# Kernel optimization log

Measured on AMD Instinct MI355X. Metric: run time of the kernel, lower is better.

Reference implementation:

```python
import jax, jax.numpy as jnp
import numpy as np

N, E, G = 50000, 800000, 64
L, C, IN, H, OUT = 3, 4, 64, 64, 64
BN_EPS = 1e-5


def setup_inputs() -> dict:
    key = jax.random.key(0)
    ks = jax.random.split(key, 12)
    x = jax.random.normal(ks[0], (N, IN), dtype=jnp.float32)
    cluster_labels = jax.random.randint(ks[1], (N,), 0, C, dtype=jnp.int32)
    edge_index = jax.random.randint(ks[2], (2, E), 0, N, dtype=jnp.int64)
    batch = jnp.sort(jax.random.randint(ks[3], (N,), 0, G, dtype=jnp.int64))
    s1 = 1.0 / np.sqrt(H)
    # per (layer, cluster) GIN MLP params: Lin(H,H) -> BN -> ReLU -> Lin(H,H)
    W1 = jax.random.normal(ks[4], (L, C, H, H), dtype=jnp.float32) * s1
    b1 = jnp.zeros((L, C, H), dtype=jnp.float32)
    g1 = jnp.ones((L, C, H), dtype=jnp.float32)
    be1 = jnp.zeros((L, C, H), dtype=jnp.float32)
    W2 = jax.random.normal(ks[5], (L, C, H, H), dtype=jnp.float32) * s1
    b2 = jnp.zeros((L, C, H), dtype=jnp.float32)
    # pool MLP: Lin(H*L, H) -> BN -> ReLU -> Lin(H, OUT)
    Wp1 = jax.random.normal(ks[6], (H * L, H), dtype=jnp.float32) / np.sqrt(H * L)
    bp1 = jnp.zeros((H,), dtype=jnp.float32)
    gp = jnp.ones((H,), dtype=jnp.float32)
    bep = jnp.zeros((H,), dtype=jnp.float32)
    Wp2 = jax.random.normal(ks[7], (H, OUT), dtype=jnp.float32) * s1
    bp2 = jnp.zeros((OUT,), dtype=jnp.float32)
    return {"x": x, "cluster_labels": cluster_labels, "edge_index": edge_index,
            "batch": batch, "W1": W1, "b1": b1, "g1": g1, "be1": be1,
            "W2": W2, "b2": b2, "Wp1": Wp1, "bp1": bp1, "gp": gp,
            "bep": bep, "Wp2": Wp2, "bp2": bp2}


def _masked_bn(h, mf, gamma, beta):
    # BatchNorm computed only over rows where mask is set (those are the rows fed to nn)
    cnt = jnp.maximum(mf.sum(), 1.0)
    mean = (mf[:, None] * h).sum(0) / cnt
    var = (mf[:, None] * (h - mean) ** 2).sum(0) / cnt
    return (h - mean) * jax.lax.rsqrt(var + BN_EPS) * gamma + beta


def _bn(h, gamma, beta):
    mean = h.mean(0)
    var = ((h - mean) ** 2).mean(0)
    return (h - mean) * jax.lax.rsqrt(var + BN_EPS) * gamma + beta


def reference(x, cluster_labels, edge_index, batch, W1, b1, g1, be1, W2, b2,
              Wp1, bp1, gp, bep, Wp2, bp2):
    src, dst = edge_index[0], edge_index[1]
    pooled = []
    for t in range(L):
        for c in range(C):
            mask = cluster_labels == c
            mf = mask.astype(x.dtype)
            # GIN aggregation: out[i] = sum_{j -> i} x[j]
            agg = jax.ops.segment_sum(x[src], dst, num_segments=N)
            h = agg + x  # (1 + eps) * x residual with eps = 0
            h = h @ W1[t, c] + b1[t, c]
            h = jax.nn.relu(_masked_bn(h, mf, g1[t, c], be1[t, c]))
            h = h @ W2[t, c] + b2[t, c]
            x = jnp.where(mask[:, None], h, x)
        pooled.append(jax.ops.segment_sum(x, batch, num_segments=G))
    z = jnp.concatenate(pooled, axis=1)  # [G, H*L]
    z = z @ Wp1 + bp1
    z = jax.nn.relu(_bn(z, gp, bep))
    return z @ Wp2 + bp2
```

## Files before the change

### kernel.cpp

```cpp
#include <hip/hip_runtime.h>
#include <hip/hip_bf16.h>

#define NN 50000
#define EE 800000
#define GG 64
#define LL 3
#define CC 4
#define HH 64
#define BN_EPS 1e-5f
#define NSHADOW 4
#define SBLK 196
#define GIN_BLOCKS 2048
#define MM_BLOCKS 256
#define ECHUNKS 3125
#define NODE_RANGE 6250
#define TMAX 2
#define H1STRIDE 80


typedef __attribute__((ext_vector_type(8))) short bf16x8;
typedef __attribute__((ext_vector_type(4))) float f32x4;

__device__ __forceinline__ float bf2f(short s) {
    return __int_as_float(((int)(unsigned short)s) << 16);
}
__device__ __forceinline__ short f2bf(float v) {
    __hip_bfloat16 hb = __float2bfloat16(v);
    return *(short*)&hb;
}


__global__ void k_deghist(const int* __restrict__ dst, int* __restrict__ deg,
                          const int* __restrict__ labels, int* __restrict__ blockcnt,
                          const float* __restrict__ x_in, __hip_bfloat16* __restrict__ xw,
                          const float* __restrict__ W1, const float* __restrict__ W2,
                          short* __restrict__ wf) {
    __shared__ int cnt[CC];
    int tid = threadIdx.x;
    for (int i = blockIdx.x * 256 + tid; i < NN * 64; i += gridDim.x * 256)
        xw[i] = __float2bfloat16(x_in[i]);
    int o = blockIdx.x * 256 + tid;
    if (o < 24 * 4096) {
        int m = o >> 12;
        int r = o & 4095;
        int colt = r >> 10;
        int fragk = (r >> 9) & 1;
        int lane = (r >> 3) & 63;
        int j = r & 7;
        int k = fragk * 32 + ((lane >> 4) << 3) + j;
        int n = colt * 16 + (lane & 15);
        const float* src = (m < 12) ? (W1 + (size_t)m * 4096) : (W2 + (size_t)(m - 12) * 4096);
        wf[o] = f2bf(src[k * 64 + n]);
    }
    bool hist = (blockIdx.x < SBLK);
    if (hist && tid < CC) cnt[tid] = 0;
    __syncthreads();
    int gid = blockIdx.x * 256 + tid;
    if (gid < EE) atomicAdd(&deg[dst[gid]], 1);
    if (hist && gid < NN) atomicAdd(&cnt[labels[gid]], 1);
    __syncthreads();
    if (hist && tid < CC) blockcnt[tid * SBLK + blockIdx.x] = cnt[tid];
}

__global__ __launch_bounds__(256) void k_scancombo(
    const int* __restrict__ deg, int* __restrict__ rowptr, int* __restrict__ dpart,
    const int* __restrict__ blockcnt, int* __restrict__ coffs, int* __restrict__ ccount) {
    __shared__ int smem[CC * 256];
    int tid = threadIdx.x;
    if (blockIdx.x < SBLK) {
        int i = blockIdx.x * 256 + tid;
        int v = (i < NN) ? deg[i] : 0;
        smem[tid] = v;
        __syncthreads();
        for (int off = 1; off < 256; off <<= 1) {
            int u = (tid >= off) ? smem[tid - off] : 0;
            __syncthreads();
            smem[tid] += u;
            __syncthreads();
        }
        if (i < NN) rowptr[i] = smem[tid] - v;
        if (tid == 255) dpart[blockIdx.x] = smem[255];
    } else {
        int own[CC];
        for (int c = 0; c < CC; c++) {
            own[c] = (tid < SBLK) ? blockcnt[c * SBLK + tid] : 0;
            smem[c * 256 + tid] = own[c];
        }
        __syncthreads();
        for (int off = 1; off < 256; off <<= 1) {
            int v[CC];
            for (int c = 0; c < CC; c++) v[c] = (tid >= off) ? smem[c * 256 + tid - off] : 0;
            __syncthreads();
            for (int c = 0; c < CC; c++) smem[c * 256 + tid] += v[c];
            __syncthreads();
        }
        if (tid < SBLK)
            for (int c = 0; c < CC; c++) coffs[c * SBLK + tid] = smem[c * 256 + tid] - own[c];
        if (tid == 0)
            for (int c = 0; c < CC; c++) ccount[c] = smem[c * 256 + 255];
    }
}

__global__ __launch_bounds__(256) void k_dscan2(int* __restrict__ dpart,
                                                int* __restrict__ dbase,
                                                int* __restrict__ rowptr) {
    __shared__ int s[256];
    int tid = threadIdx.x;
    int v = (tid < SBLK) ? dpart[tid] : 0;
    s[tid] = v;
    __syncthreads();
    for (int off = 1; off < 256; off <<= 1) {
        int u = (tid >= off) ? s[tid - off] : 0;
        __syncthreads();
        s[tid] += u;
        __syncthreads();
    }
    if (tid < SBLK) dbase[tid] = s[tid] - v;
    if (tid == 0) rowptr[NN] = EE;
}

__global__ __launch_bounds__(256) void k_cfill_dscan3(
    int* __restrict__ rowptr, const int* __restrict__ dbase, int* __restrict__ cursor,
    const int* __restrict__ labels, const int* __restrict__ coffs, int* __restrict__ clist) {
    __shared__ int pos[CC];
    int tid = threadIdx.x;
    if (tid < CC) pos[tid] = coffs[tid * SBLK + blockIdx.x];
    __syncthreads();
    int i = blockIdx.x * 256 + tid;
    if (i < NN) {
        int r = rowptr[i] + dbase[blockIdx.x];
        rowptr[i] = r;
        cursor[i] = r;
        int c = labels[i];
        int p = atomicAdd(&pos[c], 1);
        clist[c * NN + p] = i;
    }
}

__global__ void k_fill(const int* __restrict__ src, const int* __restrict__ dst,
                       int* __restrict__ cursor, int* __restrict__ adj) {
    int range = blockIdx.x / ECHUNKS;
    int e = (blockIdx.x - range * ECHUNKS) * 256 + threadIdx.x;
    if (e < EE) {
        int d = dst[e];
        int lo = range * NODE_RANGE;
        if (d >= lo && d < lo + NODE_RANGE) {
            int pos = atomicAdd(&cursor[d], 1);
            adj[pos] = src[e] << 7;
        }
    }
}

__global__ __launch_bounds__(256) void k_gather(
    const __hip_bfloat16* __restrict__ xw, const int* __restrict__ adj,
    const int* __restrict__ rowptr, const int* __restrict__ clist_c,
    const int* __restrict__ ccount_c, __hip_bfloat16* __restrict__ aggbuf,
    const int* __restrict__ batch, float* __restrict__ z, int tpool) {
    int cnt = *ccount_c;
    int lane = threadIdx.x & 63;
    int wave = threadIdx.x >> 6;
    int wid = blockIdx.x * 4 + wave;
    int nwaves = gridDim.x * 4;
    int grp = lane >> 4;
    int l16 = lane & 15;
    const char* xwb = (const char*)xw;
    int idx = wid;
    int node_next = (idx < cnt) ? clist_c[idx] : 0;
    for (; idx < cnt; idx += nwaves) {
        int node = node_next;
        int nidx = idx + nwaves;
        if (nidx < cnt) node_next = clist_c[nidx];
        int rb = rowptr[node], re = rowptr[node + 1];
        float ax[8], ay[8], az[8], aw[8];
        #pragma unroll
        for (int u = 0; u < 8; u++) { ax[u] = 0.f; ay[u] = 0.f; az[u] = 0.f; aw[u] = 0.f; }
        if (grp == 0) {
            uint2 v = *(const uint2*)(xwb + ((size_t)node << 7) + l16 * 8);
            ax[0] += __int_as_float((int)(v.x << 16));
            ay[0] += __int_as_float((int)(v.x & 0xffff0000u));
            az[0] += __int_as_float((int)(v.y << 16));
            aw[0] += __int_as_float((int)(v.y & 0xffff0000u));
        }
        int base = rb, rem = re - rb;
        while (rem > 0) {
            int take = min(rem, 64);
            int nb = adj[base + min(lane, take - 1)];
            int j = 0;
            for (; j + 32 <= take; j += 32) {
                #pragma unroll
                for (int u = 0; u < 8; u++) {
                    int o = __shfl(nb, j + u * 4 + grp);
                    uint2 v = *(const uint2*)(xwb + o + l16 * 8);
                    ax[u] += __int_as_float((int)(v.x << 16));
                    ay[u] += __int_as_float((int)(v.x & 0xffff0000u));
                    az[u] += __int_as_float((int)(v.y << 16));
                    aw[u] += __int_as_float((int)(v.y & 0xffff0000u));
                }
            }
            for (; j + 16 <= take; j += 16) {
                #pragma unroll
                for (int u = 0; u < 4; u++) {
                    int o = __shfl(nb, j + u * 4 + grp);
                    uint2 v = *(const uint2*)(xwb + o + l16 * 8);
                    ax[u] += __int_as_float((int)(v.x << 16));
                    ay[u] += __int_as_float((int)(v.x & 0xffff0000u));
                    az[u] += __int_as_float((int)(v.y << 16));
                    aw[u] += __int_as_float((int)(v.y & 0xffff0000u));
                }
            }
            for (; j < take; j += 4) {
                int e = j + grp;
                int o = __shfl(nb, min(e, take - 1));
                if (e < take) {
                    uint2 v = *(const uint2*)(xwb + o + l16 * 8);
                    ax[0] += __int_as_float((int)(v.x << 16));
                    ay[0] += __int_as_float((int)(v.x & 0xffff0000u));
                    az[0] += __int_as_float((int)(v.y << 16));
                    aw[0] += __int_as_float((int)(v.y & 0xffff0000u));
                }
            }
            base += take; rem -= take;
        }
        float X = ((ax[0] + ax[1]) + (ax[2] + ax[3])) + ((ax[4] + ax[5]) + (ax[6] + ax[7]));
        float Y = ((ay[0] + ay[1]) + (ay[2] + ay[3])) + ((ay[4] + ay[5]) + (ay[6] + ay[7]));
        float Z = ((az[0] + az[1]) + (az[2] + az[3])) + ((az[4] + az[5]) + (az[6] + az[7]));
        float W = ((aw[0] + aw[1]) + (aw[2] + aw[3])) + ((aw[4] + aw[5]) + (aw[6] + aw[7]));
        X += __shfl_xor(X, 16); X += __shfl_xor(X, 32);
        Y += __shfl_xor(Y, 16); Y += __shfl_xor(Y, 32);
        Z += __shfl_xor(Z, 16); Z += __shfl_xor(Z, 32);
        W += __shfl_xor(W, 16); W += __shfl_xor(W, 32);
        if (grp == 0) {
            ushort4 st;
            st.x = (unsigned short)f2bf(X);
            st.y = (unsigned short)f2bf(Y);
            st.z = (unsigned short)f2bf(Z);
            st.w = (unsigned short)f2bf(W);
            *(ushort4*)((char*)aggbuf + ((size_t)idx << 7) + l16 * 8) = st;
        }
    }
    if (tpool >= 0) {
        int lo = wid * 64;
        if (lo < NN) {
            int hi = min(lo + 64, NN);
            float acc = 0.f;
            int curg = batch[lo];
            for (int n = lo; n < hi; n++) {
                int g = batch[n];
                if (g != curg) {
                    atomicAdd(&z[curg * (HH * LL) + tpool * HH + lane], acc);
                    acc = 0.f;
                    curg = g;
                }
                acc += __bfloat162float(xw[(size_t)n * 64 + lane]);
            }
            atomicAdd(&z[curg * (HH * LL) + tpool * HH + lane], acc);
        }
    }
}

__global__ __launch_bounds__(256) void k_mlp(
    __hip_bfloat16* __restrict__ xw, const __hip_bfloat16* __restrict__ aggbuf,
    const int* __restrict__ clist_c, const int* __restrict__ ccount_c,
    const short* __restrict__ wf1, const float* __restrict__ b1c,
    const float* __restrict__ g1c, const float* __restrict__ be1c,
    const short* __restrict__ wf2, const float* __restrict__ b2c,
    float* __restrict__ bnacc, int* __restrict__ barcnt) {
    __shared__ __align__(16) short h1s[4 * TMAX * 16 * H1STRIDE];
    __shared__ float lds_scale[64];
    __shared__ float lds_shift[64];
    int cnt = *ccount_c;
    int tiles = (cnt + 15) >> 4;
    int lane = threadIdx.x & 63;
    int wave = threadIdx.x >> 6;
    int wid = blockIdx.x * 4 + wave;
    int nwaves = gridDim.x * 4;
    int quad = lane >> 4;
    int l15 = lane & 15;
    short* myh1 = h1s + wave * (TMAX * 16 * H1STRIDE);

    bf16x8 wb[8];
    #pragma unroll
    for (int f = 0; f < 8; f++)
        wb[f] = *(const bf16x8*)(wf1 + f * 512 + lane * 8);
    float bcol[4];
    #pragma unroll
    for (int colt = 0; colt < 4; colt++) bcol[colt] = b1c[colt * 16 + l15];

    float sS[4] = {0.f, 0.f, 0.f, 0.f};
    float sQ[4] = {0.f, 0.f, 0.f, 0.f};
    {
        int nt = 0;
        for (int tile = wid; tile < tiles && nt < TMAX; tile += nwaves, nt++) {
            int tb = tile << 4;
            int row = tb + l15;
            const __hip_bfloat16* ar = aggbuf + (size_t)row * 64 + quad * 8;
            bf16x8 a0 = *(const bf16x8*)ar;
            bf16x8 a1 = *(const bf16x8*)(ar + 32);
            short* slot = myh1 + nt * (16 * H1STRIDE);
            #pragma unroll
            for (int colt = 0; colt < 4; colt++) {
                f32x4 acc = {0.f, 0.f, 0.f, 0.f};
                acc = __builtin_amdgcn_mfma_f32_16x16x32_bf16(a0, wb[colt * 2 + 0], acc, 0, 0, 0);
                acc = __builtin_amdgcn_mfma_f32_16x16x32_bf16(a1, wb[colt * 2 + 1], acc, 0, 0, 0);
                #pragma unroll
                for (int r = 0; r < 4; r++) {
                    int nrow = tb + quad * 4 + r;
                    float s = acc[r] + bcol[colt];
                    short hb = f2bf(s);
                    slot[(quad * 4 + r) * H1STRIDE + colt * 16 + l15] = hb;
                    if (nrow < cnt) {
                        float st = bf2f(hb);
                        sS[colt] += st;
                        sQ[colt] += st * st;
                    }
                }
            }
        }
    }
    #pragma unroll
    for (int colt = 0; colt < 4; colt++) {
        sS[colt] += __shfl_xor(sS[colt], 16); sS[colt] += __shfl_xor(sS[colt], 32);
        sQ[colt] += __shfl_xor(sQ[colt], 16); sQ[colt] += __shfl_xor(sQ[colt], 32);
    }
    if (quad == 0) {
        int slot = (blockIdx.x & (NSHADOW - 1)) * 128;
        #pragma unroll
        for (int colt = 0; colt < 4; colt++) {
            atomicAdd(&bnacc[slot + colt * 16 + l15], sS[colt]);
            atomicAdd(&bnacc[slot + 64 + colt * 16 + l15], sQ[colt]);
        }
    }
    __syncthreads();
    if (threadIdx.x == 0) {
        __hip_atomic_fetch_add(barcnt, 1, __ATOMIC_RELEASE, __HIP_MEMORY_SCOPE_AGENT);
        while (__hip_atomic_load(barcnt, __ATOMIC_ACQUIRE, __HIP_MEMORY_SCOPE_AGENT) < MM_BLOCKS)
            __builtin_amdgcn_s_sleep(2);
    }
    __syncthreads();
    if (threadIdx.x < 64) {
        float s = 0.f, q = 0.f;
        #pragma unroll
        for (int sh = 0; sh < NSHADOW; sh++) {
            s += __hip_atomic_load(&bnacc[sh * 128 + threadIdx.x],
                                   __ATOMIC_RELAXED, __HIP_MEMORY_SCOPE_AGENT);
            q += __hip_atomic_load(&bnacc[sh * 128 + 64 + threadIdx.x],
                                   __ATOMIC_RELAXED, __HIP_MEMORY_SCOPE_AGENT);
        }
        float fc = fmaxf((float)cnt, 1.f);
        float mean = s / fc;
        float var = q / fc - mean * mean;
        float sc = g1c[threadIdx.x] * rsqrtf(var + BN_EPS);
        lds_scale[threadIdx.x] = sc;
        lds_shift[threadIdx.x] = be1c[threadIdx.x] - mean * sc;
    }
    __syncthreads();
    #pragma unroll
    for (int f = 0; f < 8; f++)
        wb[f] = *(const bf16x8*)(wf2 + f * 512 + lane * 8);
    #pragma unroll
    for (int colt = 0; colt < 4; colt++) bcol[colt] = b2c[colt * 16 + l15];
    float scl0[8], sft0[8], scl1[8], sft1[8];
    #pragma unroll
    for (int j = 0; j < 8; j++) {
        int ch = quad * 8 + j;
        scl0[j] = lds_scale[ch];      sft0[j] = lds_shift[ch];
        scl1[j] = lds_scale[ch + 32]; sft1[j] = lds_shift[ch + 32];
    }
    {
        int nt = 0;
        for (int tile = wid; tile < tiles && nt < TMAX; tile += nwaves, nt++) {
            int tb = tile << 4;
            const short* slot = myh1 + nt * (16 * H1STRIDE);
            const short* hr = slot + l15 * H1STRIDE + quad * 8;
            bf16x8 h0 = *(const bf16x8*)hr;
            bf16x8 h1f = *(const bf16x8*)(hr + 32);
            bf16x8 a0, a1;
            #pragma unroll
            for (int j = 0; j < 8; j++) {
                a0[j] = f2bf(fmaxf(bf2f(h0[j]) * scl0[j] + sft0[j], 0.f));
                a1[j] = f2bf(fmaxf(bf2f(h1f[j]) * scl1[j] + sft1[j], 0.f));
            }
            #pragma unroll
            for (int colt = 0; colt < 4; colt++) {
                f32x4 acc = {0.f, 0.f, 0.f, 0.f};
                acc = __builtin_amdgcn_mfma_f32_16x16x32_bf16(a0, wb[colt * 2 + 0], acc, 0, 0, 0);
                acc = __builtin_amdgcn_mfma_f32_16x16x32_bf16(a1, wb[colt * 2 + 1], acc, 0, 0, 0);
                #pragma unroll
                for (int r = 0; r < 4; r++) {
                    int nrow = tb + quad * 4 + r;
                    if (nrow < cnt) {
                        int node = clist_c[nrow];
                        xw[(size_t)node * 64 + colt * 16 + l15] =
                            __float2bfloat16(acc[r] + bcol[colt]);
                    }
                }
            }
        }
    }
}

__global__ void k_pool(const __hip_bfloat16* __restrict__ xw, const int* __restrict__ batch,
                       float* __restrict__ z, int t) {
    const int CHUNK = 64;
    int lane = threadIdx.x & 63;
    int wg = (blockIdx.x * blockDim.x + threadIdx.x) >> 6;
    int lo = wg * CHUNK;
    if (lo >= NN) return;
    int hi = min(lo + CHUNK, NN);
    float acc = 0.f;
    int curg = batch[lo];
    for (int n = lo; n < hi; n++) {
        int g = batch[n];
        if (g != curg) {
            atomicAdd(&z[curg * (HH * LL) + t * HH + lane], acc);
            acc = 0.f;
            curg = g;
        }
        acc += __bfloat162float(xw[(size_t)n * 64 + lane]);
    }
    atomicAdd(&z[curg * (HH * LL) + t * HH + lane], acc);
}

__global__ __launch_bounds__(256) void k_final1(
    const float* __restrict__ z, const float* __restrict__ Wp1,
    const float* __restrict__ bp1, float* __restrict__ hbuf) {
    __shared__ float red[256];
    int g = blockIdx.x;
    int k = threadIdx.x & 63;
    int part = threadIdx.x >> 6;
    float s = 0.f;
    #pragma unroll 8
    for (int j = part * 48; j < (part + 1) * 48; j++)
        s += z[g * (HH * LL) + j] * Wp1[j * 64 + k];
    red[threadIdx.x] = s;
    __syncthreads();
    if (part == 0)
        hbuf[g * 64 + k] = red[k] + red[64 + k] + red[128 + k] + red[192 + k] + bp1[k];
}

__global__ __launch_bounds__(256) void k_final2(
    const float* __restrict__ hbuf, const float* __restrict__ gp,
    const float* __restrict__ bep, const float* __restrict__ Wp2,
    const float* __restrict__ bp2, float* __restrict__ out) {
    __shared__ float lds[64 * 64];
    __shared__ float sscale[64];
    __shared__ float sshift[64];
    int tid = threadIdx.x;
    for (int i = tid; i < 64 * 64; i += 256) lds[i] = hbuf[i];
    __syncthreads();
    if (tid < 64) {
        float s = 0.f, q = 0.f;
        for (int g = 0; g < 64; g++) { float v = lds[g * 64 + tid]; s += v; q += v * v; }
        float mean = s / 64.f;
        float var = q / 64.f - mean * mean;
        float sc = gp[tid] * rsqrtf(var + BN_EPS);
        sscale[tid] = sc;
        sshift[tid] = bep[tid] - mean * sc;
    }
    __syncthreads();
    for (int i = tid; i < 64 * 64; i += 256) {
        int k = i & 63;
        lds[i] = fmaxf(lds[i] * sscale[k] + sshift[k], 0.f);
    }
    __syncthreads();
    for (int i = tid; i < 64 * 64; i += 256) {
        int g = i >> 6, o = i & 63;
        float s = bp2[o];
        #pragma unroll 8
        for (int k = 0; k < 64; k++) s += lds[g * 64 + k] * Wp2[k * 64 + o];
        out[g * 64 + o] = s;
    }
}

extern "C" void kernel_launch(void* const* d_in, const int* in_sizes, int n_in,
                              void* d_out, int out_size, void* d_ws, size_t ws_size,
                              hipStream_t stream) {
    const float* x_in = (const float*)d_in[0];
    const int* labels = (const int*)d_in[1];
    const int* esrc = (const int*)d_in[2];
    const int* edst = esrc + EE;
    const int* batch = (const int*)d_in[3];
    const float* W1 = (const float*)d_in[4];
    const float* b1 = (const float*)d_in[5];
    const float* g1 = (const float*)d_in[6];
    const float* be1 = (const float*)d_in[7];
    const float* W2 = (const float*)d_in[8];
    const float* b2 = (const float*)d_in[9];
    const float* Wp1 = (const float*)d_in[10];
    const float* bp1 = (const float*)d_in[11];
    const float* gp = (const float*)d_in[12];
    const float* bep = (const float*)d_in[13];
    const float* Wp2 = (const float*)d_in[14];
    const float* bp2 = (const float*)d_in[15];
    float* out = (float*)d_out;

    char* p = (char*)d_ws;
    auto carve = [&](size_t bytes) -> void* {
        void* r = (void*)p;
        p += (bytes + 255) & ~(size_t)255;
        return r;
    };
    float* bnacc = (float*)carve((size_t)LL * CC * NSHADOW * 128 * 4);
    float* z     = (float*)carve((size_t)GG * HH * LL * 4);
    int*   deg   = (int*)carve((size_t)NN * 4);
    int*   barcnt= (int*)carve((size_t)16 * 4);
    size_t zero_bytes = (size_t)(p - (char*)d_ws);
    int*   ccount  = (int*)carve(CC * 4);
    int*   blockcnt= (int*)carve((size_t)CC * SBLK * 4);
    int*   coffs   = (int*)carve((size_t)CC * SBLK * 4);
    int*   dpart   = (int*)carve((size_t)SBLK * 4);
    int*   dbase   = (int*)carve((size_t)SBLK * 4);
    __hip_bfloat16* xw     = (__hip_bfloat16*)carve((size_t)NN * 64 * 2);
    __hip_bfloat16* aggbuf = (__hip_bfloat16*)carve((size_t)NN * 64 * 2);
    short* wf      = (short*)carve((size_t)24 * 4096 * 2);
    float* hbuf    = (float*)carve((size_t)GG * 64 * 4);
    int*   rowptr  = (int*)carve((size_t)(NN + 1) * 4);
    int*   cursor  = (int*)carve((size_t)NN * 4);
    int*   adj     = (int*)carve((size_t)EE * 4);
    int*   clist   = (int*)carve((size_t)CC * NN * 4);

    hipMemsetAsync(d_ws, 0, zero_bytes, stream);

    k_deghist<<<ECHUNKS, 256, 0, stream>>>(edst, deg, labels, blockcnt, x_in, xw, W1, W2, wf);
    k_scancombo<<<SBLK + 1, 256, 0, stream>>>(deg, rowptr, dpart, blockcnt, coffs, ccount);
    k_dscan2<<<1, 256, 0, stream>>>(dpart, dbase, rowptr);
    k_cfill_dscan3<<<SBLK, 256, 0, stream>>>(rowptr, dbase, cursor, labels, coffs, clist);
    k_fill<<<ECHUNKS * 8, 256, 0, stream>>>(esrc, edst, cursor, adj);

    for (int t = 0; t < LL; t++) {
        for (int c = 0; c < CC; c++) {
            int tc = t * CC + c;
            int tpool = (c == 0) ? (t - 1) : -1;
            k_gather<<<GIN_BLOCKS, 256, 0, stream>>>(
                xw, adj, rowptr, clist + c * NN, ccount + c, aggbuf, batch, z, tpool);
            k_mlp<<<MM_BLOCKS, 256, 0, stream>>>(
                xw, aggbuf, clist + c * NN, ccount + c,
                wf + (size_t)tc * 4096, b1 + (size_t)tc * 64,
                g1 + (size_t)tc * 64, be1 + (size_t)tc * 64,
                wf + (size_t)(12 + tc) * 4096, b2 + (size_t)tc * 64,
                bnacc + (size_t)tc * NSHADOW * 128, barcnt + tc);
        }
    }
    {
        int pool_waves = (NN + 63) / 64;
        int pool_blocks = (pool_waves * 64 + 255) / 256;
        k_pool<<<pool_blocks, 256, 0, stream>>>(xw, batch, z, LL - 1);
    }
    k_final1<<<GG, 256, 0, stream>>>(z, Wp1, bp1, hbuf);
    k_final2<<<1, 256, 0, stream>>>(hbuf, gp, bep, Wp2, bp2, out);
}
```

Measured before the change: 615.6 us.

## Split fused MLP kernel at grid barrier into two launches via global h1 buffer

The fused k_mlp kernel used a software grid-wide spin barrier to finish the BatchNorm statistics before the second linear layer, and kept h1 tiles in LDS. It is now split into k_lin1, which writes h1 to a global bf16 buffer and accumulates the stats, and k_cmfma, which reads the stats and h1 back and applies BN, ReLU and the second matmul. This removes the spin-wait and the TMAX per-wave tile cap, which also drops the old requirement that all 256 blocks be co-resident. The cost is an extra kernel launch per (layer, cluster) step and an extra global write and read of h1.

```diff
diff --git a/kernel.cpp b/kernel.cpp
--- a/kernel.cpp
+++ b/kernel.cpp
@@ -14,8 +14,6 @@
 #define MM_BLOCKS 256
 #define ECHUNKS 3125
 #define NODE_RANGE 6250
-#define TMAX 2
-#define H1STRIDE 80
 
 
 typedef __attribute__((ext_vector_type(8))) short bf16x8;
@@ -258,14 +256,76 @@
     }
 }
 
-__global__ __launch_bounds__(256) void k_mlp(
-    __hip_bfloat16* __restrict__ xw, const __hip_bfloat16* __restrict__ aggbuf,
-    const int* __restrict__ clist_c, const int* __restrict__ ccount_c,
+__global__ __launch_bounds__(256) void k_lin1(
+    const __hip_bfloat16* __restrict__ aggbuf, const int* __restrict__ ccount_c,
     const short* __restrict__ wf1, const float* __restrict__ b1c,
-    const float* __restrict__ g1c, const float* __restrict__ be1c,
-    const short* __restrict__ wf2, const float* __restrict__ b2c,
-    float* __restrict__ bnacc, int* __restrict__ barcnt) {
-    __shared__ __align__(16) short h1s[4 * TMAX * 16 * H1STRIDE];
+    __hip_bfloat16* __restrict__ h1buf, float* __restrict__ bnacc) {
+    int cnt = *ccount_c;
+    int tiles = (cnt + 15) >> 4;
+    int lane = threadIdx.x & 63;
+    int wave = threadIdx.x >> 6;
+    int wid = blockIdx.x * 4 + wave;
+    int nwaves = gridDim.x * 4;
+    int quad = lane >> 4;
+    int l15 = lane & 15;
+
+    bf16x8 wb[8];
+    #pragma unroll
+    for (int f = 0; f < 8; f++)
+        wb[f] = *(const bf16x8*)(wf1 + f * 512 + lane * 8);
+    float bcol[4];
+    #pragma unroll
+    for (int colt = 0; colt < 4; colt++) bcol[colt] = b1c[colt * 16 + l15];
+
+    float sS[4] = {0.f, 0.f, 0.f, 0.f};
+    float sQ[4] = {0.f, 0.f, 0.f, 0.f};
+
+    for (int tile = wid; tile < tiles; tile += nwaves) {
+        int tb = tile << 4;
+        int row = tb + l15;
+        const __hip_bfloat16* ar = aggbuf + (size_t)row * 64 + quad * 8;
+        bf16x8 a0 = *(const bf16x8*)ar;
+        bf16x8 a1 = *(const bf16x8*)(ar + 32);
+        #pragma unroll
+        for (int colt = 0; colt < 4; colt++) {
+            f32x4 acc = {0.f, 0.f, 0.f, 0.f};
+            acc = __builtin_amdgcn_mfma_f32_16x16x32_bf16(a0, wb[colt * 2 + 0], acc, 0, 0, 0);
+            acc = __builtin_amdgcn_mfma_f32_16x16x32_bf16(a1, wb[colt * 2 + 1], acc, 0, 0, 0);
+            #pragma unroll
+            for (int r = 0; r < 4; r++) {
+                int nrow = tb + quad * 4 + r;
+                if (nrow < cnt) {
+                    float s = acc[r] + bcol[colt];
+                    __hip_bfloat16 hb = __float2bfloat16(s);
+                    h1buf[(size_t)nrow * 64 + colt * 16 + l15] = hb;
+                    float st = __bfloat162float(hb);
+                    sS[colt] += st;
+                    sQ[colt] += st * st;
+                }
+            }
+        }
+    }
+    #pragma unroll
+    for (int colt = 0; colt < 4; colt++) {
+        sS[colt] += __shfl_xor(sS[colt], 16); sS[colt] += __shfl_xor(sS[colt], 32);
+        sQ[colt] += __shfl_xor(sQ[colt], 16); sQ[colt] += __shfl_xor(sQ[colt], 32);
+    }
+    if (quad == 0) {
+        int slot = (blockIdx.x & (NSHADOW - 1)) * 128;
+        #pragma unroll
+        for (int colt = 0; colt < 4; colt++) {
+            atomicAdd(&bnacc[slot + colt * 16 + l15], sS[colt]);
+            atomicAdd(&bnacc[slot + 64 + colt * 16 + l15], sQ[colt]);
+        }
+    }
+}
+
+__global__ __launch_bounds__(256) void k_cmfma(
+    __hip_bfloat16* __restrict__ xw, const int* __restrict__ clist_c,
+    const int* __restrict__ ccount_c, const float* __restrict__ g1c,
+    const float* __restrict__ be1c, const short* __restrict__ wf2,
+    const float* __restrict__ b2c, const __hip_bfloat16* __restrict__ h1buf,
+    const float* __restrict__ bnacc) {
     __shared__ float lds_scale[64];
     __shared__ float lds_shift[64];
     int cnt = *ccount_c;
@@ -276,75 +336,13 @@
     int nwaves = gridDim.x * 4;
     int quad = lane >> 4;
     int l15 = lane & 15;
-    short* myh1 = h1s + wave * (TMAX * 16 * H1STRIDE);
-
-    bf16x8 wb[8];
-    #pragma unroll
-    for (int f = 0; f < 8; f++)
-        wb[f] = *(const bf16x8*)(wf1 + f * 512 + lane * 8);
-    float bcol[4];
-    #pragma unroll
-    for (int colt = 0; colt < 4; colt++) bcol[colt] = b1c[colt * 16 + l15];
-
-    float sS[4] = {0.f, 0.f, 0.f, 0.f};
-    float sQ[4] = {0.f, 0.f, 0.f, 0.f};
-    {
-        int nt = 0;
-        for (int tile = wid; tile < tiles && nt < TMAX; tile += nwaves, nt++) {
-            int tb = tile << 4;
-            int row = tb + l15;
-            const __hip_bfloat16* ar = aggbuf + (size_t)row * 64 + quad * 8;
-            bf16x8 a0 = *(const bf16x8*)ar;
-            bf16x8 a1 = *(const bf16x8*)(ar + 32);
-            short* slot = myh1 + nt * (16 * H1STRIDE);
-            #pragma unroll
-            for (int colt = 0; colt < 4; colt++) {
-                f32x4 acc = {0.f, 0.f, 0.f, 0.f};
-                acc = __builtin_amdgcn_mfma_f32_16x16x32_bf16(a0, wb[colt * 2 + 0], acc, 0, 0, 0);
-                acc = __builtin_amdgcn_mfma_f32_16x16x32_bf16(a1, wb[colt * 2 + 1], acc, 0, 0, 0);
-                #pragma unroll
-                for (int r = 0; r < 4; r++) {
-                    int nrow = tb + quad * 4 + r;
-                    float s = acc[r] + bcol[colt];
-                    short hb = f2bf(s);
-                    slot[(quad * 4 + r) * H1STRIDE + colt * 16 + l15] = hb;
-                    if (nrow < cnt) {
-                        float st = bf2f(hb);
-                        sS[colt] += st;
-                        sQ[colt] += st * st;
-                    }
-                }
-            }
-        }
-    }
-    #pragma unroll
-    for (int colt = 0; colt < 4; colt++) {
-        sS[colt] += __shfl_xor(sS[colt], 16); sS[colt] += __shfl_xor(sS[colt], 32);
-        sQ[colt] += __shfl_xor(sQ[colt], 16); sQ[colt] += __shfl_xor(sQ[colt], 32);
-    }
-    if (quad == 0) {
-        int slot = (blockIdx.x & (NSHADOW - 1)) * 128;
-        #pragma unroll
-        for (int colt = 0; colt < 4; colt++) {
-            atomicAdd(&bnacc[slot + colt * 16 + l15], sS[colt]);
-            atomicAdd(&bnacc[slot + 64 + colt * 16 + l15], sQ[colt]);
-        }
-    }
-    __syncthreads();
-    if (threadIdx.x == 0) {
-        __hip_atomic_fetch_add(barcnt, 1, __ATOMIC_RELEASE, __HIP_MEMORY_SCOPE_AGENT);
-        while (__hip_atomic_load(barcnt, __ATOMIC_ACQUIRE, __HIP_MEMORY_SCOPE_AGENT) < MM_BLOCKS)
-            __builtin_amdgcn_s_sleep(2);
-    }
-    __syncthreads();
+
     if (threadIdx.x < 64) {
         float s = 0.f, q = 0.f;
         #pragma unroll
         for (int sh = 0; sh < NSHADOW; sh++) {
-            s += __hip_atomic_load(&bnacc[sh * 128 + threadIdx.x],
-                                   __ATOMIC_RELAXED, __HIP_MEMORY_SCOPE_AGENT);
-            q += __hip_atomic_load(&bnacc[sh * 128 + 64 + threadIdx.x],
-                                   __ATOMIC_RELAXED, __HIP_MEMORY_SCOPE_AGENT);
+            s += bnacc[sh * 128 + threadIdx.x];
+            q += bnacc[sh * 128 + 64 + threadIdx.x];
         }
         float fc = fmaxf((float)cnt, 1.f);
         float mean = s / fc;
@@ -354,9 +352,12 @@
         lds_shift[threadIdx.x] = be1c[threadIdx.x] - mean * sc;
     }
     __syncthreads();
+
+    bf16x8 wb[8];
     #pragma unroll
     for (int f = 0; f < 8; f++)
         wb[f] = *(const bf16x8*)(wf2 + f * 512 + lane * 8);
+    float bcol[4];
     #pragma unroll
     for (int colt = 0; colt < 4; colt++) bcol[colt] = b2c[colt * 16 + l15];
     float scl0[8], sft0[8], scl1[8], sft1[8];
@@ -366,33 +367,31 @@
         scl0[j] = lds_scale[ch];      sft0[j] = lds_shift[ch];
         scl1[j] = lds_scale[ch + 32]; sft1[j] = lds_shift[ch + 32];
     }
-    {
-        int nt = 0;
-        for (int tile = wid; tile < tiles && nt < TMAX; tile += nwaves, nt++) {
-            int tb = tile << 4;
-            const short* slot = myh1 + nt * (16 * H1STRIDE);
-            const short* hr = slot + l15 * H1STRIDE + quad * 8;
-            bf16x8 h0 = *(const bf16x8*)hr;
-            bf16x8 h1f = *(const bf16x8*)(hr + 32);
-            bf16x8 a0, a1;
+
+    for (int tile = wid; tile < tiles; tile += nwaves) {
+        int tb = tile << 4;
+        int row = tb + l15;
+        const __hip_bfloat16* hr = h1buf + (size_t)row * 64 + quad * 8;
+        bf16x8 h0 = *(const bf16x8*)hr;
+        bf16x8 h1f = *(const bf16x8*)(hr + 32);
+        bf16x8 a0, a1;
+        #pragma unroll
+        for (int j = 0; j < 8; j++) {
+            a0[j] = f2bf(fmaxf(bf2f(h0[j]) * scl0[j] + sft0[j], 0.f));
+            a1[j] = f2bf(fmaxf(bf2f(h1f[j]) * scl1[j] + sft1[j], 0.f));
+        }
+        #pragma unroll
+        for (int colt = 0; colt < 4; colt++) {
+            f32x4 acc = {0.f, 0.f, 0.f, 0.f};
+            acc = __builtin_amdgcn_mfma_f32_16x16x32_bf16(a0, wb[colt * 2 + 0], acc, 0, 0, 0);
+            acc = __builtin_amdgcn_mfma_f32_16x16x32_bf16(a1, wb[colt * 2 + 1], acc, 0, 0, 0);
             #pragma unroll
-            for (int j = 0; j < 8; j++) {
-                a0[j] = f2bf(fmaxf(bf2f(h0[j]) * scl0[j] + sft0[j], 0.f));
-                a1[j] = f2bf(fmaxf(bf2f(h1f[j]) * scl1[j] + sft1[j], 0.f));
-            }
-            #pragma unroll
-            for (int colt = 0; colt < 4; colt++) {
-                f32x4 acc = {0.f, 0.f, 0.f, 0.f};
-                acc = __builtin_amdgcn_mfma_f32_16x16x32_bf16(a0, wb[colt * 2 + 0], acc, 0, 0, 0);
-                acc = __builtin_amdgcn_mfma_f32_16x16x32_bf16(a1, wb[colt * 2 + 1], acc, 0, 0, 0);
-                #pragma unroll
-                for (int r = 0; r < 4; r++) {
-                    int nrow = tb + quad * 4 + r;
-                    if (nrow < cnt) {
-                        int node = clist_c[nrow];
-                        xw[(size_t)node * 64 + colt * 16 + l15] =
-                            __float2bfloat16(acc[r] + bcol[colt]);
-                    }
+            for (int r = 0; r < 4; r++) {
+                int nrow = tb + quad * 4 + r;
+                if (nrow < cnt) {
+                    int node = clist_c[nrow];
+                    xw[(size_t)node * 64 + colt * 16 + l15] =
+                        __float2bfloat16(acc[r] + bcol[colt]);
                 }
             }
         }
@@ -503,7 +502,6 @@
     float* bnacc = (float*)carve((size_t)LL * CC * NSHADOW * 128 * 4);
     float* z     = (float*)carve((size_t)GG * HH * LL * 4);
     int*   deg   = (int*)carve((size_t)NN * 4);
-    int*   barcnt= (int*)carve((size_t)16 * 4);
     size_t zero_bytes = (size_t)(p - (char*)d_ws);
     int*   ccount  = (int*)carve(CC * 4);
     int*   blockcnt= (int*)carve((size_t)CC * SBLK * 4);
@@ -512,6 +510,7 @@
     int*   dbase   = (int*)carve((size_t)SBLK * 4);
     __hip_bfloat16* xw     = (__hip_bfloat16*)carve((size_t)NN * 64 * 2);
     __hip_bfloat16* aggbuf = (__hip_bfloat16*)carve((size_t)NN * 64 * 2);
+    __hip_bfloat16* h1buf  = (__hip_bfloat16*)carve((size_t)NN * 64 * 2);
     short* wf      = (short*)carve((size_t)24 * 4096 * 2);
     float* hbuf    = (float*)carve((size_t)GG * 64 * 4);
     int*   rowptr  = (int*)carve((size_t)(NN + 1) * 4);
@@ -533,12 +532,14 @@
             int tpool = (c == 0) ? (t - 1) : -1;
             k_gather<<<GIN_BLOCKS, 256, 0, stream>>>(
                 xw, adj, rowptr, clist + c * NN, ccount + c, aggbuf, batch, z, tpool);
-            k_mlp<<<MM_BLOCKS, 256, 0, stream>>>(
-                xw, aggbuf, clist + c * NN, ccount + c,
-                wf + (size_t)tc * 4096, b1 + (size_t)tc * 64,
+            k_lin1<<<MM_BLOCKS, 256, 0, stream>>>(
+                aggbuf, ccount + c, wf + (size_t)tc * 4096, b1 + (size_t)tc * 64,
+                h1buf, bnacc + (size_t)tc * NSHADOW * 128);
+            k_cmfma<<<MM_BLOCKS, 256, 0, stream>>>(
+                xw, clist + c * NN, ccount + c,
                 g1 + (size_t)tc * 64, be1 + (size_t)tc * 64,
                 wf + (size_t)(12 + tc) * 4096, b2 + (size_t)tc * 64,
-                bnacc + (size_t)tc * NSHADOW * 128, barcnt + tc);
+                h1buf, bnacc + (size_t)tc * NSHADOW * 128);
         }
     }
     {
```

Measured after the change: 560.5 us. 9.0% less time.
